# Performance work log

Hardware: AMD Instinct MI355X
Metric: run time of the kernel (lower is better)

The kernel has to match this reference:

```python
import jax, jax.numpy as jnp
import numpy as np
from jax import lax

DT = 0.05
EPS = 1e-4


def _mlp_sp(W1, b1, W2, b2, x):
    # 2->4->1 MLP with tanh, then softplus + eps (SDEFunc.f / SDEFunc.g)
    h = jnp.tanh(x @ W1 + b1)
    return jax.nn.softplus(h @ W2 + b2) + EPS


def setup_inputs() -> dict:
    key = jax.random.key(0)
    ks = jax.random.split(key, 10)
    T, N = 2001, 16384
    ts = jnp.arange(T, dtype=jnp.float32) * DT  # grid spaced exactly dt=0.05
    x0 = jax.random.uniform(ks[0], (1,), dtype=jnp.float32)
    noise = jax.random.normal(ks[1], (T - 1, N, 1), dtype=jnp.float32)
    s1 = 1.0 / np.sqrt(2.0)
    s2 = 1.0 / np.sqrt(4.0)
    Wf1 = jax.random.normal(ks[2], (2, 4), dtype=jnp.float32) * s1
    bf1 = jnp.zeros((4,), dtype=jnp.float32)
    Wf2 = jax.random.normal(ks[3], (4, 1), dtype=jnp.float32) * s2
    bf2 = jnp.zeros((1,), dtype=jnp.float32)
    Wg1 = jax.random.normal(ks[4], (2, 4), dtype=jnp.float32) * s1
    bg1 = jnp.zeros((4,), dtype=jnp.float32)
    Wg2 = jax.random.normal(ks[5], (4, 1), dtype=jnp.float32) * s2
    bg2 = jnp.zeros((1,), dtype=jnp.float32)
    return {"ts": ts, "x0": x0, "noise": noise,
            "Wf1": Wf1, "bf1": bf1, "Wf2": Wf2, "bf2": bf2,
            "Wg1": Wg1, "bg1": bg1, "Wg2": Wg2, "bg2": bg2}


def reference(ts, x0, noise, Wf1, bf1, Wf2, bf2, Wg1, bg1, Wg2, bg2):
    N = noise.shape[1]
    x_init = jnp.broadcast_to(x0.reshape(1, 1), (N, 1))  # [N,1] state
    dts = jnp.diff(ts)  # [T-1], equals dt=0.05 on this grid

    def step(x, inp):
        t, dt, z = inp
        tcol = jnp.broadcast_to(t, (x.shape[0], 1))
        xt = jnp.concatenate([x, tcol], axis=-1)  # [N,2]
        f = _mlp_sp(Wf1, bf1, Wf2, bf2, xt)       # drift, [N,1]
        g = _mlp_sp(Wg1, bg1, Wg2, bg2, xt)       # diagonal diffusion, [N,1]
        x_new = x + f * dt + g * jnp.sqrt(dt) * z
        return x_new, x_new

    _, xs = lax.scan(step, x_init, (ts[:-1], dts, noise))  # [T-1,N,1]
    xs_full = jnp.concatenate([x_init[None], xs], axis=0)   # [T,N,1]
    # original returns np.stack over N trajectories of [T] paths -> [N,T]
    return jnp.transpose(xs_full[:, :, 0])
```

## Files before the change

kernel.cpp:

```cpp
#include <hip/hip_runtime.h>

#define EPSV  1e-4f
#define LOG2E 1.44269504088896341f
#define LN2   0.69314718055994531f
#define TSC   (2.0f * LOG2E)

typedef float v2f __attribute__((ext_vector_type(2)));

constexpr int CH = 16;

__device__ __forceinline__ float dpp_xor1(float v) {
    int i = __builtin_bit_cast(int, v);
    i = __builtin_amdgcn_update_dpp(i, i, 0xB1, 0xF, 0xF, false);
    return __builtin_bit_cast(float, i);
}
__device__ __forceinline__ float dpp_xor2(float v) {
    int i = __builtin_bit_cast(int, v);
    i = __builtin_amdgcn_update_dpp(i, i, 0x4E, 0xF, 0xF, false);
    return __builtin_bit_cast(float, i);
}
template<int IMM>
__device__ __forceinline__ float qbcast(float v) {
    int i = __builtin_bit_cast(int, v);
    i = __builtin_amdgcn_update_dpp(i, i, IMM, 0xF, 0xF, false);
    return __builtin_bit_cast(float, i);
}
__device__ __forceinline__ float qbg(int g, float v) {
    switch (g) {
    case 0:  return qbcast<0x00>(v);
    case 1:  return qbcast<0x55>(v);
    case 2:  return qbcast<0xAA>(v);
    default: return qbcast<0xFF>(v);
    }
}

__global__ __launch_bounds__(256)
__attribute__((amdgpu_waves_per_eu(1, 1)))
void sde_quad_kernel(
    const float* __restrict__ noise,
    const float* __restrict__ x0,
    const float* __restrict__ Wf1, const float* __restrict__ bf1,
    const float* __restrict__ Wf2, const float* __restrict__ bf2,
    const float* __restrict__ Wg1, const float* __restrict__ bg1,
    const float* __restrict__ Wg2, const float* __restrict__ bg2,
    float* __restrict__ out, int N, int T)
{
    const int tid = blockIdx.x * blockDim.x + threadIdx.x;
    const int n = tid >> 2;
    const int r = tid & 3;
    if (n >= N) return;
    const int steps = T - 1;
    const bool isf = (r < 2);

    const float* W1 = isf ? Wf1 : Wg1;
    const float* B1 = isf ? bf1 : bg1;
    const float* W2 = isf ? Wf2 : Wg2;
    const float* B2 = isf ? bf2 : bg2;
    const int j0 = (r & 1) * 2;

    const v2f w1x2 = { W1[j0] * TSC,     W1[j0 + 1] * TSC };
    const v2f w1t2 = { W1[4 + j0] * TSC, W1[5 + j0] * TSC };
    const v2f b12  = { B1[j0] * TSC,     B1[j0 + 1] * TSC };
    const float w2a = W2[j0] * LOG2E, w2b = W2[j0 + 1] * LOG2E;
    const float b2h = B2[0] * LOG2E * 0.5f;
    const float w2a2 = -2.0f * w2a, w2b2 = -2.0f * w2b;
    const float Kc   = w2a + w2b + b2h;

    float x = x0[0];
    float* __restrict__ outp = out;
    if (r == 0) outp[(unsigned)n * (unsigned)T] = x;

    float zA[4], zB[4];
    v2f   cab[CH];
    float c1v[CH], c0v[CH];

    const int nfull = steps / CH;
    const unsigned uN = (unsigned)N;
    const unsigned lanebase = (unsigned)n + (unsigned)(4 * r) * uN;
    unsigned obase = (unsigned)n * (unsigned)T + 1;
    float vstore = x;
    float kfb = 0.0f;
    float tcarry = 0.0f;

    auto PREF = [&](float (&zb)[4], int cc) {
        if (cc < nfull) {
            const unsigned b = lanebase + (unsigned)(cc * CH) * uN;
            zb[0] = noise[b];
            zb[1] = noise[b + uN];
            zb[2] = noise[b + 2u * uN];
            zb[3] = noise[b + 3u * uN];
        }
    };

    auto PREP16 = [&](const float (&zb)[4]) {
        float tpv = tcarry;
        #pragma unroll
        for (int i = 0; i < CH; ++i) {
            const float kfi = kfb + (float)(i + 1);
            const float tn  = kfi * 0.05f;
            const float dtk = tn - tpv;
            const float sdt = __builtin_amdgcn_sqrtf(dtk);
            cab[i] = w1t2 * tpv + b12;
            const float z   = qbg(i >> 2, zb[i & 3]);
            const float mz  = sdt * z;
            const float mm  = isf ? dtk : mz;
            c1v[i] = LN2  * mm;
            c0v[i] = EPSV * mm;
            tpv = tn;
        }
        tcarry = tpv;
        kfb += 16.0f;
    };

    auto CHAIN16 = [&]() {
        #pragma unroll
        for (int i = 0; i < CH; ++i) {
            const v2f  s   = w1x2 * x + cab[i];
            const v2f  ev  = { __builtin_amdgcn_exp2f(s.x), __builtin_amdgcn_exp2f(s.y) };
            const v2f  e1  = ev + 1.0f;
            const float ra = __builtin_amdgcn_rcpf(e1.x);
            const float rb = __builtin_amdgcn_rcpf(e1.y);
            const float pd = fmaf(w2a2, ra, fmaf(w2b2, rb, Kc));
            const float y2 = pd + dpp_xor1(pd);
            const float u  = __builtin_amdgcn_exp2f(y2);
            const float lg = __builtin_amdgcn_logf(1.0f + u);
            const float d  = fmaf(lg, c1v[i], c0v[i]);
            x = (x + d) + dpp_xor2(d);
            vstore = ((i & 3) == r) ? x : vstore;
            if ((i & 3) == 3) { outp[obase + (unsigned)r] = vstore; obase += 4u; }
        }
    };

    if (nfull > 0) PREF(zA, 0);

    int c = 0;
    while (c + 2 <= nfull) {
        PREF(zB, c + 1);
        PREP16(zA);
        CHAIN16();
        PREF(zA, c + 2);
        PREP16(zB);
        CHAIN16();
        c += 2;
    }
    if (c < nfull) {
        PREP16(zA);
        CHAIN16();
        ++c;
    }

    {
        float kf = kfb, tc = tcarry;
        for (int k = nfull * CH; k < steps; ++k) {
            const float z   = noise[(unsigned)k * uN + (unsigned)n];
            kf += 1.0f;
            const float tn  = kf * 0.05f;
            const float dtk = tn - tc;
            const float sdt = __builtin_amdgcn_sqrtf(dtk);
            const v2f  cabt = w1t2 * tc + b12;
            const float mz  = sdt * z;
            const float mm  = isf ? dtk : mz;
            const float c1  = LN2  * mm;
            const float c0  = EPSV * mm;
            const v2f  s    = w1x2 * x + cabt;
            const v2f  ev   = { __builtin_amdgcn_exp2f(s.x), __builtin_amdgcn_exp2f(s.y) };
            const v2f  e1   = ev + 1.0f;
            const float ra  = __builtin_amdgcn_rcpf(e1.x);
            const float rb  = __builtin_amdgcn_rcpf(e1.y);
            const float pd  = fmaf(w2a2, ra, fmaf(w2b2, rb, Kc));
            const float y2  = pd + dpp_xor1(pd);
            const float u   = __builtin_amdgcn_exp2f(y2);
            const float lg  = __builtin_amdgcn_logf(1.0f + u);
            const float d   = fmaf(lg, c1, c0);
            x = (x + d) + dpp_xor2(d);
            if (r == 0) outp[(unsigned)n * (unsigned)T + (unsigned)(k + 1)] = x;
            tc = tn;
        }
    }
}

extern "C" void kernel_launch(void* const* d_in, const int* in_sizes, int n_in,
                              void* d_out, int out_size, void* d_ws, size_t ws_size,
                              hipStream_t stream) {
    const float* ts    = (const float*)d_in[0]; (void)ts;
    const float* x0    = (const float*)d_in[1];
    const float* noise = (const float*)d_in[2];
    const float* Wf1   = (const float*)d_in[3];
    const float* bf1   = (const float*)d_in[4];
    const float* Wf2   = (const float*)d_in[5];
    const float* bf2   = (const float*)d_in[6];
    const float* Wg1   = (const float*)d_in[7];
    const float* bg1   = (const float*)d_in[8];
    const float* Wg2   = (const float*)d_in[9];
    const float* bg2   = (const float*)d_in[10];

    const int T = in_sizes[0];
    const int N = (T > 1) ? in_sizes[2] / (T - 1) : 0;
    float* out = (float*)d_out;

    const int threads = N * 4;
    const int block = 256;
    const int grid = (threads + block - 1) / block;
    hipLaunchKernelGGL(sde_quad_kernel, dim3(grid), dim3(block), 0, stream,
                       noise, x0, Wf1, bf1, Wf2, bf2, Wg1, bg1, Wg2, bg2, out, N, T);
}
```

Before: 165.8 us.

## Interleave next-chunk coefficient prep with current chain and precompute sqrt(dt) table

Each 16-step chain step is now interleaved with preparation of the next chunk's coefficients, so independent prep arithmetic can fill latency gaps in the serial transcendental chain. A small setup kernel writes sqrt(dt) per step into workspace, and the main kernel loads it per lane and multiplies it into the noise before the quad broadcast, instead of computing sqrt for every step. This adds an extra kernel launch and extra loads and registers, and keeps a fallback path when no workspace is available.

```diff
diff --git a/kernel.cpp b/kernel.cpp
--- a/kernel.cpp
+++ b/kernel.cpp
@@ -34,6 +34,16 @@
     }
 }
 
+__global__ __launch_bounds__(256) void sde_sdt_setup(float* __restrict__ sdtt, int steps)
+{
+    int k = blockIdx.x * blockDim.x + threadIdx.x;
+    if (k >= steps) return;
+    const float t0 = (float)k * 0.05f;
+    const float t1 = (float)(k + 1) * 0.05f;
+    sdtt[k] = __builtin_amdgcn_sqrtf(t1 - t0);
+}
+
+template<bool TBL>
 __global__ __launch_bounds__(256)
 __attribute__((amdgpu_waves_per_eu(1, 1)))
 void sde_quad_kernel(
@@ -43,6 +53,7 @@
     const float* __restrict__ Wf2, const float* __restrict__ bf2,
     const float* __restrict__ Wg1, const float* __restrict__ bg1,
     const float* __restrict__ Wg2, const float* __restrict__ bg2,
+    const float* __restrict__ sdtt,
     float* __restrict__ out, int N, int T)
 {
     const int tid = blockIdx.x * blockDim.x + threadIdx.x;
@@ -70,7 +81,7 @@
     float* __restrict__ outp = out;
     if (r == 0) outp[(unsigned)n * (unsigned)T] = x;
 
-    float zA[4], zB[4];
+    float zP[4], zQ[4], sP[4], sQ[4];
     v2f   cab[CH];
     float c1v[CH], c0v[CH];
 
@@ -80,77 +91,108 @@
     unsigned obase = (unsigned)n * (unsigned)T + 1;
     float vstore = x;
     float kfb = 0.0f;
-    float tcarry = 0.0f;
-
-    auto PREF = [&](float (&zb)[4], int cc) {
+
+    auto PREFZ = [&](float (&zb)[4], float (&sb)[4], int cc) {
         if (cc < nfull) {
             const unsigned b = lanebase + (unsigned)(cc * CH) * uN;
             zb[0] = noise[b];
             zb[1] = noise[b + uN];
             zb[2] = noise[b + 2u * uN];
             zb[3] = noise[b + 3u * uN];
-        }
-    };
-
-    auto PREP16 = [&](const float (&zb)[4]) {
-        float tpv = tcarry;
+            if constexpr (TBL) {
+                const unsigned tb = (unsigned)(cc * CH + 4 * r);
+                sb[0] = sdtt[tb];
+                sb[1] = sdtt[tb + 1];
+                sb[2] = sdtt[tb + 2];
+                sb[3] = sdtt[tb + 3];
+            }
+        }
+    };
+
+    auto PREP_STEP = [&](int i, const float (&mzo)[4]) {
+        const float kfp = kfb + (float)i;
+        const float tp  = kfp * 0.05f;
+        const float tn  = (kfb + (float)(i + 1)) * 0.05f;
+        const float dtk = tn - tp;
+        cab[i] = w1t2 * tp + b12;
+        const float mzq = qbg(i >> 2, mzo[i & 3]);
+        float mm;
+        if constexpr (TBL) {
+            mm = isf ? dtk : mzq;
+        } else {
+            mm = isf ? dtk : __builtin_amdgcn_sqrtf(dtk) * mzq;
+        }
+        c1v[i] = LN2  * mm;
+        c0v[i] = EPSV * mm;
+    };
+
+    auto CHAIN_STEP = [&](int i) {
+        const v2f  s   = w1x2 * x + cab[i];
+        const v2f  ev  = { __builtin_amdgcn_exp2f(s.x), __builtin_amdgcn_exp2f(s.y) };
+        const v2f  e1  = ev + 1.0f;
+        const float ra = __builtin_amdgcn_rcpf(e1.x);
+        const float rb = __builtin_amdgcn_rcpf(e1.y);
+        const float pd = fmaf(w2a2, ra, fmaf(w2b2, rb, Kc));
+        const float y2 = pd + dpp_xor1(pd);
+        const float u  = __builtin_amdgcn_exp2f(y2);
+        const float lg = __builtin_amdgcn_logf(1.0f + u);
+        const float d  = fmaf(lg, c1v[i], c0v[i]);
+        x = (x + d) + dpp_xor2(d);
+        vstore = ((i & 3) == r) ? x : vstore;
+        if ((i & 3) == 3) { outp[obase + (unsigned)r] = vstore; obase += 4u; }
+    };
+
+    auto FUSED = [&](const float (&zr)[4], const float (&sr)[4],
+                     float (&zf)[4], float (&sf)[4], int prefcc) {
+        PREFZ(zf, sf, prefcc);
+        float mzo[4];
+        #pragma unroll
+        for (int j = 0; j < 4; ++j) {
+            if constexpr (TBL) mzo[j] = zr[j] * sr[j];
+            else               mzo[j] = zr[j];
+        }
         #pragma unroll
         for (int i = 0; i < CH; ++i) {
-            const float kfi = kfb + (float)(i + 1);
-            const float tn  = kfi * 0.05f;
-            const float dtk = tn - tpv;
-            const float sdt = __builtin_amdgcn_sqrtf(dtk);
-            cab[i] = w1t2 * tpv + b12;
-            const float z   = qbg(i >> 2, zb[i & 3]);
-            const float mz  = sdt * z;
-            const float mm  = isf ? dtk : mz;
-            c1v[i] = LN2  * mm;
-            c0v[i] = EPSV * mm;
-            tpv = tn;
-        }
-        tcarry = tpv;
+            CHAIN_STEP(i);
+            PREP_STEP(i, mzo);
+        }
         kfb += 16.0f;
     };
 
     auto CHAIN16 = [&]() {
         #pragma unroll
-        for (int i = 0; i < CH; ++i) {
-            const v2f  s   = w1x2 * x + cab[i];
-            const v2f  ev  = { __builtin_amdgcn_exp2f(s.x), __builtin_amdgcn_exp2f(s.y) };
-            const v2f  e1  = ev + 1.0f;
-            const float ra = __builtin_amdgcn_rcpf(e1.x);
-            const float rb = __builtin_amdgcn_rcpf(e1.y);
-            const float pd = fmaf(w2a2, ra, fmaf(w2b2, rb, Kc));
-            const float y2 = pd + dpp_xor1(pd);
-            const float u  = __builtin_amdgcn_exp2f(y2);
-            const float lg = __builtin_amdgcn_logf(1.0f + u);
-            const float d  = fmaf(lg, c1v[i], c0v[i]);
-            x = (x + d) + dpp_xor2(d);
-            vstore = ((i & 3) == r) ? x : vstore;
-            if ((i & 3) == 3) { outp[obase + (unsigned)r] = vstore; obase += 4u; }
-        }
-    };
-
-    if (nfull > 0) PREF(zA, 0);
+        for (int i = 0; i < CH; ++i) CHAIN_STEP(i);
+    };
+
+    if (nfull > 0) {
+        PREFZ(zQ, sQ, 0);
+        float mzo[4];
+        #pragma unroll
+        for (int j = 0; j < 4; ++j) {
+            if constexpr (TBL) mzo[j] = zQ[j] * sQ[j];
+            else               mzo[j] = zQ[j];
+        }
+        #pragma unroll
+        for (int i = 0; i < CH; ++i) PREP_STEP(i, mzo);
+        kfb += 16.0f;
+        PREFZ(zP, sP, 1);
+    }
 
     int c = 0;
-    while (c + 2 <= nfull) {
-        PREF(zB, c + 1);
-        PREP16(zA);
-        CHAIN16();
-        PREF(zA, c + 2);
-        PREP16(zB);
-        CHAIN16();
+    while (c + 2 <= nfull - 1) {
+        FUSED(zP, sP, zQ, sQ, c + 2);
+        FUSED(zQ, sQ, zP, sP, c + 3);
         c += 2;
     }
-    if (c < nfull) {
-        PREP16(zA);
-        CHAIN16();
+    if (c <= nfull - 2) {
+        FUSED(zP, sP, zQ, sQ, c + 2);
         ++c;
     }
+    if (nfull > 0) CHAIN16();
 
     {
-        float kf = kfb, tc = tcarry;
+        float kf = kfb;
+        float tc = kf * 0.05f;
         for (int k = nfull * CH; k < steps; ++k) {
             const float z   = noise[(unsigned)k * uN + (unsigned)n];
             kf += 1.0f;
@@ -158,8 +200,7 @@
             const float dtk = tn - tc;
             const float sdt = __builtin_amdgcn_sqrtf(dtk);
             const v2f  cabt = w1t2 * tc + b12;
-            const float mz  = sdt * z;
-            const float mm  = isf ? dtk : mz;
+            const float mm  = isf ? dtk : sdt * z;
             const float c1  = LN2  * mm;
             const float c0  = EPSV * mm;
             const v2f  s    = w1x2 * x + cabt;
@@ -196,11 +237,26 @@
 
     const int T = in_sizes[0];
     const int N = (T > 1) ? in_sizes[2] / (T - 1) : 0;
+    const int steps = T - 1;
     float* out = (float*)d_out;
 
     const int threads = N * 4;
     const int block = 256;
     const int grid = (threads + block - 1) / block;
-    hipLaunchKernelGGL(sde_quad_kernel, dim3(grid), dim3(block), 0, stream,
-                       noise, x0, Wf1, bf1, Wf2, bf2, Wg1, bg1, Wg2, bg2, out, N, T);
-}
+
+    const bool use_tbl = (steps > 0) && (d_ws != nullptr) &&
+                         (ws_size >= (size_t)steps * sizeof(float));
+
+    if (use_tbl) {
+        const int sgrid = (steps + block - 1) / block;
+        hipLaunchKernelGGL(sde_sdt_setup, dim3(sgrid), dim3(block), 0, stream,
+                           (float*)d_ws, steps);
+        hipLaunchKernelGGL((sde_quad_kernel<true>), dim3(grid), dim3(block), 0, stream,
+                           noise, x0, Wf1, bf1, Wf2, bf2, Wg1, bg1, Wg2, bg2,
+                           (const float*)d_ws, out, N, T);
+    } else {
+        hipLaunchKernelGGL((sde_quad_kernel<false>), dim3(grid), dim3(block), 0, stream,
+                           noise, x0, Wf1, bf1, Wf2, bf2, Wg1, bg1, Wg2, bg2,
+                           (const float*)nullptr, out, N, T);
+    }
+}
```

Result: slower. 178.8 us (+7.9%).
